# Optimization experiments

Hardware: AMD Instinct MI355X
Metric: run time of the kernel (lower is better)

Reference implementation:

```python
import jax, jax.numpy as jnp
import numpy as np

B, S, D = 2, 4096, 1024
H, HD = 16, 64
M = 512              # memseqlen == chunk size
L = 2 * M            # memory + chunk tokens
HID = 2816
EPS = 1e-5


def setup_inputs() -> dict:
    key = jax.random.key(0)
    ks = jax.random.split(key, 16)
    sc = 0.02
    return {
        "x": jax.random.normal(ks[0], (B, S, D), jnp.float32),
        "freqs_cos": jax.random.uniform(ks[1], (L, HD // 2), jnp.float32),
        "freqs_sin": jax.random.uniform(ks[2], (L, HD // 2), jnp.float32),
        "wq": jax.random.normal(ks[3], (D, D), jnp.float32) * sc,
        "wk": jax.random.normal(ks[4], (D, D), jnp.float32) * sc,
        "wv": jax.random.normal(ks[5], (D, D), jnp.float32) * sc,
        "wo": jax.random.normal(ks[6], (D, D), jnp.float32) * sc,
        "wm": jax.random.normal(ks[7], (D, D), jnp.float32) * sc,
        "wkm": jax.random.normal(ks[8], (D, D), jnp.float32) * sc,
        "wvm": jax.random.normal(ks[9], (D, D), jnp.float32) * sc,
        "w1": jax.random.normal(ks[10], (D, HID), jnp.float32) * sc,
        "w3": jax.random.normal(ks[11], (D, HID), jnp.float32) * sc,
        "w2": jax.random.normal(ks[12], (HID, D), jnp.float32) * sc,
        "ffn_norm_w": jnp.ones((D,), jnp.float32),
        "mem_norm_w": jnp.ones((D,), jnp.float32),
        "origin_mem": jnp.zeros((1, M, D), jnp.float32),
    }


def _rmsnorm(x, w):
    return x * jax.lax.rsqrt(jnp.mean(x * x, axis=-1, keepdims=True) + EPS) * w


def _rope(t, cos, sin):
    # t: (B, L, H, HD); cos/sin: (L, HD//2). Adjacent-pair complex rotation (llama2.c style).
    tr = t.reshape(*t.shape[:-1], HD // 2, 2)
    t_r, t_i = tr[..., 0], tr[..., 1]
    c = cos[None, :, None, :]
    s = sin[None, :, None, :]
    o_r = t_r * c - t_i * s
    o_i = t_r * s + t_i * c
    return jnp.stack([o_r, o_i], axis=-1).reshape(t.shape)


def reference(x, freqs_cos, freqs_sin, wq, wk, wv, wo, wm, wkm, wvm,
              w1, w2, w3, ffn_norm_w, mem_norm_w, origin_mem):
    bsz = x.shape[0]
    cos = freqs_cos[:L]
    sin = freqs_sin[:L]
    causal = jnp.tril(jnp.ones((L, L), dtype=bool))
    scale = 1.0 / jnp.sqrt(jnp.asarray(HD, x.dtype))

    def ffn(h):
        return (jax.nn.silu(h @ w1) * (h @ w3)) @ w2

    def step(om, subx):
        # token projections
        xq = (subx @ wq).reshape(bsz, M, H, HD)
        xk = (subx @ wk).reshape(bsz, M, H, HD)
        xv = (subx @ wv).reshape(bsz, M, H, HD)
        # memory glue: wm -> ffn residual -> rmsnorm
        om2 = om @ wm
        om2 = om2 + ffn(_rmsnorm(om2, ffn_norm_w))
        om2 = _rmsnorm(om2, mem_norm_w)
        # memory projections (source bug: mq is overwritten by mk; wqm unused)
        mk = (om2 @ wkm).reshape(bsz, M, H, HD)
        mv = (om2 @ wvm).reshape(bsz, M, H, HD)
        mq = mk
        q = jnp.concatenate([mq, xq], axis=1)  # (B, L, H, HD)
        k = jnp.concatenate([mk, xk], axis=1)
        v = jnp.concatenate([mv, xv], axis=1)
        q = _rope(q, cos, sin)
        k = _rope(k, cos, sin)
        # SDPA, causal over the concatenated length (n_rep == 1, repeat_kv is identity)
        qh = q.transpose(0, 2, 1, 3)
        kh = k.transpose(0, 2, 1, 3)
        vh = v.transpose(0, 2, 1, 3)
        scores = jnp.einsum('bhqd,bhkd->bhqk', qh, kh) * scale
        scores = jnp.where(causal, scores, jnp.finfo(scores.dtype).min)
        attn = jax.nn.softmax(scores, axis=-1)
        out = jnp.einsum('bhqk,bhkd->bhqd', attn, vh)
        out = out.transpose(0, 2, 1, 3).reshape(bsz, L, D)
        om_new = out[:, M:]  # token-part becomes next memory AND this chunk's output
        return om_new, om_new

    om0 = jnp.broadcast_to(origin_mem, (bsz, M, D))
    xc = x.reshape(bsz, S // M, M, D).transpose(1, 0, 2, 3)  # (n_chunks, B, M, D)
    _, outs = jax.lax.scan(step, om0, xc)
    out = outs.transpose(1, 0, 2, 3).reshape(bsz, S, D)
    return out @ wo
```

## Files before the change

### kernel.cpp

```cpp
#include <hip/hip_runtime.h>
#include <hip/hip_bf16.h>


#define D_    1024
#define H_    16
#define HD_   64
#define M_    512
#define L_    1024
#define HID_  2816
#define NSTEP 8

typedef __hip_bfloat16 bf16;
typedef _Float16 f16;
typedef __attribute__((ext_vector_type(8))) short short8;
typedef __attribute__((ext_vector_type(8))) _Float16 f16x8;
typedef __attribute__((ext_vector_type(4))) _Float16 f16x4;
typedef __attribute__((ext_vector_type(2))) _Float16 f16x2;
typedef __attribute__((ext_vector_type(4))) float floatx4;

__global__ void probe_dtype(const void* x, int* flag) {
  int lane = threadIdx.x;
  unsigned short v = ((const unsigned short*)x)[2 * lane];
  int e = (v >> 7) & 0xFF;
  bool sane = (e >= 100 && e <= 140);
  unsigned long long m = __ballot(sane);
  if (lane == 0) flag[0] = (__popcll(m) >= 40) ? 1 : 0;
}

__device__ __forceinline__ float load_any(const void* p, long i, int isbf) {
  return isbf ? __bfloat162float(((const bf16*)p)[i]) : ((const float*)p)[i];
}

__global__ __launch_bounds__(256) void transpose_cast(const void* in, bf16* out,
                                                      int K, int N, const int* flagp,
                                                      int stride, int off) {
  __shared__ float tile[32][33];
  int isbf = flagp[0];
  int tx = threadIdx.x & 31, ty = threadIdx.x >> 5;
  int n = blockIdx.x * 32 + tx;
#pragma unroll
  for (int i = 0; i < 4; i++) {
    int k = blockIdx.y * 32 + ty + i * 8;
    tile[ty + i * 8][tx] = load_any(in, (long)k * N + n, isbf);
  }
  __syncthreads();
  int k2 = blockIdx.y * 32 + tx;
#pragma unroll
  for (int i = 0; i < 4; i++) {
    int n2 = blockIdx.x * 32 + ty + i * 8;
    out[((long)n2 * stride + off) * K + k2] = __float2bfloat16(tile[tx][ty + i * 8]);
  }
}

__global__ __launch_bounds__(256) void transpose_cast_d7(
    const void* wq, const void* wk, const void* wv, const void* wm,
    const void* wkm, const void* wvm, const void* wo,
    bf16* wqkvT, bf16* wmT, bf16* wkmvmT, bf16* woT, const int* flagp) {
  __shared__ float tile[32][33];
  int z = blockIdx.z;
  const void* in;
  bf16* out;
  switch (z) {
    case 0: in = wq;  out = wqkvT;               break;
    case 1: in = wk;  out = wqkvT + 1048576;     break;
    case 2: in = wv;  out = wqkvT + 2 * 1048576; break;
    case 3: in = wm;  out = wmT;                 break;
    case 4: in = wkm; out = wkmvmT;              break;
    case 5: in = wvm; out = wkmvmT + 1048576;    break;
    default: in = wo; out = woT;                 break;
  }
  int isbf = flagp[0];
  int tx = threadIdx.x & 31, ty = threadIdx.x >> 5;
  int n = blockIdx.x * 32 + tx;
#pragma unroll
  for (int i = 0; i < 4; i++) {
    int k = blockIdx.y * 32 + ty + i * 8;
    tile[ty + i * 8][tx] = load_any(in, (long)k * 1024 + n, isbf);
  }
  __syncthreads();
  int k2 = blockIdx.y * 32 + tx;
#pragma unroll
  for (int i = 0; i < 4; i++) {
    int n2 = blockIdx.x * 32 + ty + i * 8;
    out[(long)n2 * 1024 + k2] = __float2bfloat16(tile[tx][ty + i * 8]);
  }
}

__global__ __launch_bounds__(256) void cast_to_bf16(const void* in, bf16* out, int n,
                                                    const int* flagp) {
  int i = blockIdx.x * 256 + threadIdx.x;
  if (i < n) out[i] = __float2bfloat16(load_any(in, i, flagp[0]));
}

__global__ __launch_bounds__(256) void cast_to_f32(const void* in, float* out, int n,
                                                   const int* flagp) {
  int i = blockIdx.x * 256 + threadIdx.x;
  if (i < n) out[i] = load_any(in, i, flagp[0]);
}

__global__ __launch_bounds__(256) void init_om(const void* in, bf16* om, const int* flagp) {
  int i = blockIdx.x * 256 + threadIdx.x;
  int rem = i & (M_ * D_ - 1);
  om[i] = __float2bfloat16(load_any(in, rem, flagp[0]));
}

#define GEMM64_BODY(Aptr, WTptr, Kld, kbeg, kend)                                   \
  __shared__ char smem[16384];                                                      \
  char* aT = smem;                                                                  \
  char* bT = smem + 8192;                                                           \
  int tid = threadIdx.x;                                                            \
  int wave = tid >> 6, lane = tid & 63;                                             \
  int wm_ = wave >> 1, wn_ = wave & 1;                                              \
  floatx4 acc[2][2] = {};                                                           \
  int q0 = tid, q1 = tid + 256;                                                     \
  int am0 = q0 >> 3, ac0 = q0 & 7;                                                  \
  int am1 = q1 >> 3, ac1 = q1 & 7;                                                  \
  long grow0 = R0 + am0, grow1 = R0 + am1;                                          \
  long bn0 = (long)(C0 + am0) * (Kld), bn1 = (long)(C0 + am1) * (Kld);              \
  int lofa0 = (am0 * 8 + (ac0 ^ (am0 & 7))) * 16;                                   \
  int lofa1 = (am1 * 8 + (ac1 ^ (am1 & 7))) * 16;                                   \
  for (int k0 = (kbeg); k0 < (kend); k0 += 64) {                                    \
    uint4 va0 = *(const uint4*)((Aptr) + grow0 * (Kld) + k0 + ac0 * 8);             \
    uint4 va1 = *(const uint4*)((Aptr) + grow1 * (Kld) + k0 + ac1 * 8);             \
    uint4 vb0 = *(const uint4*)((WTptr) + bn0 + k0 + ac0 * 8);                      \
    uint4 vb1 = *(const uint4*)((WTptr) + bn1 + k0 + ac1 * 8);                      \
    __syncthreads();                                                                \
    *(uint4*)(aT + lofa0) = va0;                                                    \
    *(uint4*)(aT + lofa1) = va1;                                                    \
    *(uint4*)(bT + lofa0) = vb0;                                                    \
    *(uint4*)(bT + lofa1) = vb1;                                                    \
    __syncthreads();                                                                \
    _Pragma("unroll") for (int kki = 0; kki < 2; ++kki) {                           \
      int cbase = kki * 4 + (lane >> 4);                                            \
      short8 af[2], bfr[2];                                                         \
      _Pragma("unroll") for (int i = 0; i < 2; ++i) {                               \
        int ml = wm_ * 32 + i * 16 + (lane & 15);                                   \
        af[i] = *(const short8*)(aT + (ml * 8 + (cbase ^ (ml & 7))) * 16);          \
        int nl = wn_ * 32 + i * 16 + (lane & 15);                                   \
        bfr[i] = *(const short8*)(bT + (nl * 8 + (cbase ^ (nl & 7))) * 16);         \
      }                                                                             \
      _Pragma("unroll") for (int i = 0; i < 2; ++i)                                 \
          _Pragma("unroll") for (int j = 0; j < 2; ++j) acc[i][j] =                 \
              __builtin_amdgcn_mfma_f32_16x16x32_bf16(af[i], bfr[j], acc[i][j],     \
                                                      0, 0, 0);                     \
    }                                                                               \
  }

__global__ __launch_bounds__(256) void gemm64_sk(
    const bf16* __restrict__ A, const bf16* __restrict__ WT,
    float* __restrict__ outP, int N, int Kfull, int Ksplit) {
  int C0 = blockIdx.x * 64, R0 = blockIdx.y * 64;
  int kb = blockIdx.z;
  float* out = outP + ((size_t)kb << 20);
  int kbeg = kb * Ksplit;
  GEMM64_BODY(A, WT, Kfull, kbeg, kbeg + Ksplit)
#pragma unroll
  for (int i = 0; i < 2; ++i)
#pragma unroll
    for (int j = 0; j < 2; ++j) {
      int row = R0 + wm_ * 32 + i * 16 + (lane >> 4) * 4;
      int col = C0 + wn_ * 32 + j * 16 + (lane & 15);
#pragma unroll
      for (int rg = 0; rg < 4; ++rg)
        out[(long)(row + rg) * N + col] = acc[i][j][rg];
    }
}

__global__ __launch_bounds__(256) void gemm64_kmvm(
    const bf16* __restrict__ A, const bf16* __restrict__ WT,
    const float* __restrict__ cosf, const float* __restrict__ sinf,
    f16* __restrict__ k_mem, f16* __restrict__ v_memT) {
  int C0 = blockIdx.x * 64, R0 = blockIdx.y * 64;
  GEMM64_BODY(A, WT, 1024, 0, 1024)
#pragma unroll
  for (int i = 0; i < 2; ++i)
#pragma unroll
    for (int j = 0; j < 2; ++j) {
      int row0 = R0 + wm_ * 32 + i * 16 + (lane >> 4) * 4;
      int col = C0 + wn_ * 32 + j * 16 + (lane & 15);
#pragma unroll
      for (int rg = 0; rg < 4; ++rg) {
        float v = acc[i][j][rg];
        int row = row0 + rg;
        int b = row >> 9, pos = row & 511;
        if (C0 < 1024) {
          float partner = __shfl_xor(v, 1);
          int ii = (col & 63) >> 1;
          float c = cosf[pos * 32 + ii], s = sinf[pos * 32 + ii];
          float o = (col & 1) ? (partner * s + v * c) : (v * c - partner * s);
          int bh = b * 16 + ((col >> 6) & 15);
          k_mem[((size_t)bh * 512 + pos) * 64 + (col & 63)] = (f16)o;
        } else {
          int d = col & 63;
          int bh = b * 16 + ((col - 1024) >> 6);
          v_memT[((size_t)bh * 64 + d) * 512 + pos] = (f16)v;
        }
      }
    }
}

__global__ __launch_bounds__(256) void gemm128(
    const bf16* __restrict__ A, const bf16* __restrict__ WT,
    void* __restrict__ out, const int* __restrict__ flagp,
    int N, int K, int out_mode,
    const float* __restrict__ cosf, const float* __restrict__ sinf,
    f16* __restrict__ q_x, f16* __restrict__ k_x, f16* __restrict__ v_xT) {
  __shared__ char smem[32768];
  int tid = threadIdx.x;
  int w = tid >> 6, lane = tid & 63;
  int C0 = blockIdx.x * 128, R0 = blockIdx.y * 128;
  int wm = (w >> 1) * 64, wn = (w & 1) * 64;
  int g = lane >> 4, n16 = lane & 15;
  floatx4 acc[4][4] = {};
  int lr = lane >> 3, lc = lane & 7;

  for (int k0 = 0; k0 < K; k0 += 64) {
    __syncthreads();
#pragma unroll
    for (int i = 0; i < 4; ++i) {
      int m = w * 32 + i * 8 + lr;
      int cg = lc ^ (m & 7);
      const bf16* ga = A + (size_t)(R0 + m) * K + k0 + cg * 8;
      const bf16* gb = WT + (size_t)(C0 + m) * K + k0 + cg * 8;
      __builtin_amdgcn_global_load_lds(
          (const __attribute__((address_space(1))) void*)ga,
          (__attribute__((address_space(3))) void*)(smem + (w * 32 + i * 8) * 128),
          16, 0, 0);
      __builtin_amdgcn_global_load_lds(
          (const __attribute__((address_space(1))) void*)gb,
          (__attribute__((address_space(3))) void*)(smem + 16384 + (w * 32 + i * 8) * 128),
          16, 0, 0);
    }
    __syncthreads();
#pragma unroll
    for (int kk = 0; kk < 2; ++kk) {
      short8 af[4], bfr[4];
#pragma unroll
      for (int i = 0; i < 4; ++i) {
        int ml = wm + i * 16 + n16;
        af[i] = *(const short8*)(smem + (ml * 8 + ((kk * 4 + g) ^ (ml & 7))) * 16);
        int nl = wn + i * 16 + n16;
        bfr[i] = *(const short8*)(smem + 16384 + (nl * 8 + ((kk * 4 + g) ^ (nl & 7))) * 16);
      }
#pragma unroll
      for (int i = 0; i < 4; ++i)
#pragma unroll
        for (int j = 0; j < 4; ++j)
          acc[i][j] = __builtin_amdgcn_mfma_f32_16x16x32_bf16(af[i], bfr[j], acc[i][j], 0, 0, 0);
    }
  }
  int isbf = flagp ? flagp[0] : 0;
#pragma unroll
  for (int i = 0; i < 4; ++i)
#pragma unroll
    for (int j = 0; j < 4; ++j) {
      int row = R0 + wm + i * 16 + g * 4;
      int col = C0 + wn + j * 16 + n16;
      if (out_mode == 4) {
        if (col < 2048) {
#pragma unroll
          for (int rg = 0; rg < 4; ++rg) {
            float v = acc[i][j][rg];
            float partner = __shfl_xor(v, 1);
            int r = row + rg;
            int m = r & 511, t = (r >> 9) & 7, b = r >> 12;
            int pos = 512 + m;
            int ii = (col & 63) >> 1;
            float c = cosf[pos * 32 + ii], s = sinf[pos * 32 + ii];
            float o = (col & 1) ? (partner * s + v * c) : (v * c - partner * s);
            int h = (col >> 6) & 15;
            size_t slab = (size_t)t * 32 + b * 16 + h;
            if (col < 1024)
              q_x[(slab * 512 + m) * 64 + (col & 63)] = (f16)(o * 0.125f);
            else
              k_x[(slab * 512 + m) * 64 + (col & 63)] = (f16)o;
          }
        } else {
          int r = row;
          int m = r & 511, t = (r >> 9) & 7, b = r >> 12;
          int d = col & 63, h = (col - 2048) >> 6;
          size_t slab = (size_t)t * 32 + b * 16 + h;
          f16x4 vv;
#pragma unroll
          for (int rg = 0; rg < 4; ++rg) vv[rg] = (f16)acc[i][j][rg];
          *(f16x4*)(v_xT + (slab * 64 + d) * 512 + m) = vv;
        }
        continue;
      }
#pragma unroll
      for (int rg = 0; rg < 4; ++rg) {
        float v = acc[i][j][rg];
        if (out_mode == 3) {
          float partner = __shfl_xor(v, 1);
          if ((n16 & 1) == 0) {
            float a = v;
            float s = a / (1.f + __expf(-a));
            ((bf16*)out)[(long)(row + rg) * HID_ + (col >> 1)] =
                __float2bfloat16(s * partner);
          }
          continue;
        }
        long off = (long)(row + rg) * N + col;
        if (out_mode == 0) ((float*)out)[off] = v;
        else if (out_mode == 1) ((f16*)out)[off] = (f16)v;
        else {
          if (isbf) ((bf16*)out)[off] = __float2bfloat16(v);
          else ((float*)out)[off] = v;
        }
      }
    }
}

__global__ __launch_bounds__(256) void rmsnorm_cast(const float* __restrict__ X,
                                                    const float* __restrict__ Wn,
                                                    bf16* __restrict__ Y,
                                                    const float* __restrict__ P,
                                                    int np,
                                                    float* __restrict__ sumout) {
  int row = blockIdx.x, tid = threadIdx.x;
  float vals[4], ss = 0.f;
#pragma unroll
  for (int i = 0; i < 4; i++) {
    int c = tid + i * 256;
    long idx = (long)row * D_ + c;
    float v = X ? X[idx] : 0.f;
    for (int k = 0; k < np; ++k) v += P[((size_t)k << 20) + idx];
    vals[i] = v;
    ss += v * v;
  }
#pragma unroll
  for (int off = 32; off; off >>= 1) ss += __shfl_xor(ss, off);
  __shared__ float wsum[4];
  int wv = tid >> 6, lane = tid & 63;
  if (lane == 0) wsum[wv] = ss;
  __syncthreads();
  ss = wsum[0] + wsum[1] + wsum[2] + wsum[3];
  float r = rsqrtf(ss * (1.0f / D_) + 1e-5f);
#pragma unroll
  for (int i = 0; i < 4; i++) {
    int c = tid + i * 256;
    if (sumout) sumout[(long)row * D_ + c] = vals[i];
    Y[(long)row * D_ + c] = __float2bfloat16(vals[i] * r * Wn[c]);
  }
}

__global__ __launch_bounds__(256) void attn_x(
    const f16* __restrict__ q_x, const f16* __restrict__ k_x,
    const f16* __restrict__ v_xT, float* __restrict__ OpartX,
    float* __restrict__ mpartX, float* __restrict__ lpartX) {
  __shared__ char smem[40960];
  int qt = blockIdx.x, bh = blockIdx.y, t = blockIdx.z;
  int tid = threadIdx.x;
  int w = tid >> 6, lane = tid & 63;
  int g = lane >> 4, n16 = lane & 15;
  int numc = qt + 1;
  int pos = 512 + qt * 64 + w * 16 + n16;
  size_t slab = (size_t)t * 32 + bh;

  f16x8 qf[2];
  {
    const f16* qp = q_x + (slab * 512 + qt * 64 + w * 16 + n16) * 64 + g * 8;
    qf[0] = *(const f16x8*)(qp);
    qf[1] = *(const f16x8*)(qp + 32);
  }
  floatx4 O[4] = {};
  float mrun = -1e30f, lrun = 0.f;

  int id0 = tid, id1 = tid + 256;
  int r0 = id0 >> 3, cc0 = id0 & 7;
  int r1 = id1 >> 3, cc1 = id1 & 7;
  int lof0 = ((r0 << 3) | (cc0 ^ (r0 & 7))) * 16;
  int lof1 = ((r1 << 3) | (cc1 ^ (r1 & 7))) * 16;

  uint4 kv0 = *(const uint4*)(k_x + (slab * 512 + r0) * 64 + cc0 * 8);
  uint4 kv1 = *(const uint4*)(k_x + (slab * 512 + r1) * 64 + cc1 * 8);
  uint4 vv0 = *(const uint4*)(v_xT + (slab * 64 + r0) * 512 + cc0 * 8);
  uint4 vv1 = *(const uint4*)(v_xT + (slab * 64 + r1) * 512 + cc1 * 8);

  char* Pw = smem + 32768 + w * 2048;

  for (int c = 0; c < numc; ++c) {
    char* Kb = smem + (c & 1) * 8192;
    char* Vb = smem + 16384 + (c & 1) * 8192;
    *(uint4*)(Kb + lof0) = kv0;
    *(uint4*)(Kb + lof1) = kv1;
    *(uint4*)(Vb + lof0) = vv0;
    *(uint4*)(Vb + lof1) = vv1;
    if (c + 1 < numc) {
      int ca = c + 1;
      kv0 = *(const uint4*)(k_x + (slab * 512 + ca * 64 + r0) * 64 + cc0 * 8);
      kv1 = *(const uint4*)(k_x + (slab * 512 + ca * 64 + r1) * 64 + cc1 * 8);
      vv0 = *(const uint4*)(v_xT + (slab * 64 + r0) * 512 + ca * 64 + cc0 * 8);
      vv1 = *(const uint4*)(v_xT + (slab * 64 + r1) * 512 + ca * 64 + cc1 * 8);
    }
    __syncthreads();

    floatx4 S[4] = {};
    __builtin_amdgcn_s_setprio(1);
#pragma unroll
    for (int kk = 0; kk < 2; ++kk) {
#pragma unroll
      for (int tn = 0; tn < 4; ++tn) {
        int row = tn * 16 + n16;
        f16x8 kf = *(const f16x8*)(Kb + (((row << 3) | ((kk * 4 + g) ^ (row & 7))) * 16));
        S[tn] = __builtin_amdgcn_mfma_f32_16x16x32_f16(kf, qf[kk], S[tn], 0, 0, 0);
      }
    }
    __builtin_amdgcn_s_setprio(0);
    if (c == numc - 1) {
      int kb = 512 + qt * 64;
#pragma unroll
      for (int tn = 0; tn < 4; ++tn)
#pragma unroll
        for (int r = 0; r < 4; ++r) {
          int key = kb + tn * 16 + g * 4 + r;
          if (key > pos) S[tn][r] = -1e30f;
        }
    }
    float smax = -1e30f;
#pragma unroll
    for (int tn = 0; tn < 4; ++tn)
#pragma unroll
      for (int r = 0; r < 4; ++r) smax = fmaxf(smax, S[tn][r]);
    smax = fmaxf(smax, __shfl_xor(smax, 16));
    smax = fmaxf(smax, __shfl_xor(smax, 32));
    float corr = 1.f;
    if (__any(smax > mrun + 8.f)) {
      float newm = fmaxf(mrun, smax);
      corr = __expf(mrun - newm);
      mrun = newm;
      float cr[4];
#pragma unroll
      for (int r = 0; r < 4; ++r) cr[r] = __shfl(corr, g * 4 + r);
#pragma unroll
      for (int dt = 0; dt < 4; ++dt)
#pragma unroll
        for (int r = 0; r < 4; ++r) O[dt][r] *= cr[r];
    }
    float lsum = 0.f;
#pragma unroll
    for (int tn = 0; tn < 4; ++tn) {
      f16x4 pk;
#pragma unroll
      for (int r = 0; r < 4; ++r) {
        float p = __expf(S[tn][r] - mrun);
        lsum += p;
        pk[r] = (f16)p;
      }
      int kapb = tn * 16 + g * 4;
      *(f16x4*)(Pw + (((n16 << 3) | ((kapb >> 3) ^ (n16 & 7))) * 16 + (kapb & 7) * 2)) = pk;
    }
    lsum += __shfl_xor(lsum, 16);
    lsum += __shfl_xor(lsum, 32);
    lrun = lrun * corr + lsum;
    __builtin_amdgcn_s_setprio(1);
#pragma unroll
    for (int kk = 0; kk < 2; ++kk) {
      f16x8 pf = *(const f16x8*)(Pw + (((n16 << 3) | ((kk * 4 + g) ^ (n16 & 7))) * 16));
#pragma unroll
      for (int dt = 0; dt < 4; ++dt) {
        int row = dt * 16 + n16;
        f16x8 vf =
            *(const f16x8*)(Vb + (((row << 3) | ((kk * 4 + g) ^ (row & 7))) * 16));
        O[dt] = __builtin_amdgcn_mfma_f32_16x16x32_f16(pf, vf, O[dt], 0, 0, 0);
      }
    }
    __builtin_amdgcn_s_setprio(0);
    __syncthreads();
  }
  int b = bh >> 4, h = bh & 15;
  if (g == 0) {
    int qq = qt * 64 + w * 16 + n16;
    mpartX[(size_t)t * 16384 + bh * 512 + qq] = mrun;
    lpartX[(size_t)t * 16384 + bh * 512 + qq] = lrun;
  }
#pragma unroll
  for (int dt = 0; dt < 4; ++dt)
#pragma unroll
    for (int r = 0; r < 4; ++r) {
      int qq = qt * 64 + w * 16 + g * 4 + r;
      size_t col = (size_t)h * 64 + dt * 16 + n16;
      OpartX[((size_t)t << 20) + (size_t)(b * 512 + qq) * 1024 + col] = O[dt][r];
    }
}

__global__ __launch_bounds__(256) void attn_mem(
    const f16* __restrict__ q_x, const f16* __restrict__ k_mem,
    const f16* __restrict__ v_memT, const float* __restrict__ OX,
    const float* __restrict__ mX, const float* __restrict__ lX,
    bf16* __restrict__ om_bf, bf16* __restrict__ outs_bf, int t) {
  __shared__ char smem[40960];
  int qt = blockIdx.x, bh = blockIdx.y;
  int tid = threadIdx.x;
  int w = tid >> 6, lane = tid & 63;
  int g = lane >> 4, n16 = lane & 15;
  size_t slab = (size_t)t * 32 + bh;

  f16x8 qf[2];
  {
    const f16* qp = q_x + (slab * 512 + qt * 64 + w * 16 + n16) * 64 + g * 8;
    qf[0] = *(const f16x8*)(qp);
    qf[1] = *(const f16x8*)(qp + 32);
  }
  floatx4 O[4] = {};
  float mrun = -1e30f, lrun = 0.f;

  int id0 = tid, id1 = tid + 256;
  int r0 = id0 >> 3, cc0 = id0 & 7;
  int r1 = id1 >> 3, cc1 = id1 & 7;
  int lof0 = ((r0 << 3) | (cc0 ^ (r0 & 7))) * 16;
  int lof1 = ((r1 << 3) | (cc1 ^ (r1 & 7))) * 16;

  uint4 kv0 = *(const uint4*)(k_mem + ((size_t)bh * 512 + r0) * 64 + cc0 * 8);
  uint4 kv1 = *(const uint4*)(k_mem + ((size_t)bh * 512 + r1) * 64 + cc1 * 8);
  uint4 vv0 = *(const uint4*)(v_memT + ((size_t)bh * 64 + r0) * 512 + cc0 * 8);
  uint4 vv1 = *(const uint4*)(v_memT + ((size_t)bh * 64 + r1) * 512 + cc1 * 8);

  char* Pw = smem + 32768 + w * 2048;

  for (int c = 0; c < 8; ++c) {
    char* Kb = smem + (c & 1) * 8192;
    char* Vb = smem + 16384 + (c & 1) * 8192;
    *(uint4*)(Kb + lof0) = kv0;
    *(uint4*)(Kb + lof1) = kv1;
    *(uint4*)(Vb + lof0) = vv0;
    *(uint4*)(Vb + lof1) = vv1;
    if (c + 1 < 8) {
      int ca = c + 1;
      kv0 = *(const uint4*)(k_mem + ((size_t)bh * 512 + ca * 64 + r0) * 64 + cc0 * 8);
      kv1 = *(const uint4*)(k_mem + ((size_t)bh * 512 + ca * 64 + r1) * 64 + cc1 * 8);
      vv0 = *(const uint4*)(v_memT + ((size_t)bh * 64 + r0) * 512 + ca * 64 + cc0 * 8);
      vv1 = *(const uint4*)(v_memT + ((size_t)bh * 64 + r1) * 512 + ca * 64 + cc1 * 8);
    }
    __syncthreads();

    floatx4 S[4] = {};
    __builtin_amdgcn_s_setprio(1);
#pragma unroll
    for (int kk = 0; kk < 2; ++kk) {
#pragma unroll
      for (int tn = 0; tn < 4; ++tn) {
        int row = tn * 16 + n16;
        f16x8 kf = *(const f16x8*)(Kb + (((row << 3) | ((kk * 4 + g) ^ (row & 7))) * 16));
        S[tn] = __builtin_amdgcn_mfma_f32_16x16x32_f16(kf, qf[kk], S[tn], 0, 0, 0);
      }
    }
    __builtin_amdgcn_s_setprio(0);
    float smax = -1e30f;
#pragma unroll
    for (int tn = 0; tn < 4; ++tn)
#pragma unroll
      for (int r = 0; r < 4; ++r) smax = fmaxf(smax, S[tn][r]);
    smax = fmaxf(smax, __shfl_xor(smax, 16));
    smax = fmaxf(smax, __shfl_xor(smax, 32));
    float corr = 1.f;
    if (__any(smax > mrun + 8.f)) {
      float newm = fmaxf(mrun, smax);
      corr = __expf(mrun - newm);
      mrun = newm;
      float cr[4];
#pragma unroll
      for (int r = 0; r < 4; ++r) cr[r] = __shfl(corr, g * 4 + r);
#pragma unroll
      for (int dt = 0; dt < 4; ++dt)
#pragma unroll
        for (int r = 0; r < 4; ++r) O[dt][r] *= cr[r];
    }
    float lsum = 0.f;
#pragma unroll
    for (int tn = 0; tn < 4; ++tn) {
      f16x4 pk;
#pragma unroll
      for (int r = 0; r < 4; ++r) {
        float p = __expf(S[tn][r] - mrun);
        lsum += p;
        pk[r] = (f16)p;
      }
      int kapb = tn * 16 + g * 4;
      *(f16x4*)(Pw + (((n16 << 3) | ((kapb >> 3) ^ (n16 & 7))) * 16 + (kapb & 7) * 2)) = pk;
    }
    lsum += __shfl_xor(lsum, 16);
    lsum += __shfl_xor(lsum, 32);
    lrun = lrun * corr + lsum;
    __builtin_amdgcn_s_setprio(1);
#pragma unroll
    for (int kk = 0; kk < 2; ++kk) {
      f16x8 pf = *(const f16x8*)(Pw + (((n16 << 3) | ((kk * 4 + g) ^ (n16 & 7))) * 16));
#pragma unroll
      for (int dt = 0; dt < 4; ++dt) {
        int row = dt * 16 + n16;
        f16x8 vf =
            *(const f16x8*)(Vb + (((row << 3) | ((kk * 4 + g) ^ (row & 7))) * 16));
        O[dt] = __builtin_amdgcn_mfma_f32_16x16x32_f16(pf, vf, O[dt], 0, 0, 0);
      }
    }
    __builtin_amdgcn_s_setprio(0);
    __syncthreads();
  }
  int b = bh >> 4, h = bh & 15;
  float a1[4], a2[4], rden[4];
  int qqr[4];
#pragma unroll
  for (int r = 0; r < 4; ++r) {
    float m1 = __shfl(mrun, g * 4 + r);
    float l1 = __shfl(lrun, g * 4 + r);
    qqr[r] = qt * 64 + w * 16 + g * 4 + r;
    int idx = bh * 512 + qqr[r];
    float m2 = mX[idx], l2 = lX[idx];
    float Mx = fmaxf(m1, m2);
    a1[r] = __expf(m1 - Mx);
    a2[r] = __expf(m2 - Mx);
    rden[r] = 1.f / (a1[r] * l1 + a2[r] * l2);
  }
#pragma unroll
  for (int dt = 0; dt < 4; ++dt)
#pragma unroll
    for (int r = 0; r < 4; ++r) {
      size_t col = (size_t)h * 64 + dt * 16 + n16;
      size_t rowoff = (size_t)(b * 512 + qqr[r]) * 1024 + col;
      float o2 = OX[rowoff];
      float v = (a1[r] * O[dt][r] + a2[r] * o2) * rden[r];
      bf16 bv = __float2bfloat16(v);
      om_bf[rowoff] = bv;
      outs_bf[((size_t)(b * 4096 + t * 512 + qqr[r])) * 1024 + col] = bv;
    }
}

extern "C" void kernel_launch(void* const* d_in, const int* in_sizes, int n_in,
                              void* d_out, int out_size, void* d_ws, size_t ws_size,
                              hipStream_t stream) {
  (void)in_sizes; (void)n_in; (void)out_size; (void)ws_size;
  const void* x   = d_in[0];
  const void* fc  = d_in[1];
  const void* fs  = d_in[2];
  const void* wq  = d_in[3];
  const void* wk  = d_in[4];
  const void* wv  = d_in[5];
  const void* wo  = d_in[6];
  const void* wm  = d_in[7];
  const void* wkm = d_in[8];
  const void* wvm = d_in[9];
  const void* w1  = d_in[10];
  const void* w3  = d_in[11];
  const void* w2  = d_in[12];
  const void* fnw = d_in[13];
  const void* mnw = d_in[14];
  const void* om0 = d_in[15];

  char* p = (char*)d_ws;
  auto alloc = [&](size_t bytes) -> char* {
    char* r = p;
    p += (bytes + 255) & ~(size_t)255;
    return r;
  };
  int*   flag    = (int*)alloc(256);
  bf16*  wqkvT   = (bf16*)alloc((size_t)3 * 1048576 * 2);
  bf16*  wmT     = (bf16*)alloc((size_t)1048576 * 2);
  bf16*  wkmvmT  = (bf16*)alloc((size_t)2 * 1048576 * 2);
  bf16*  w13T    = (bf16*)alloc((size_t)2 * 2883584 * 2);
  bf16*  w2T     = (bf16*)alloc((size_t)2883584 * 2);
  bf16*  woT     = (bf16*)alloc((size_t)1048576 * 2);
  bf16*  xb      = (bf16*)alloc((size_t)8388608 * 2);
  float* cosf    = (float*)alloc((size_t)32768 * 4);
  float* sinf    = (float*)alloc((size_t)32768 * 4);
  float* ffnw    = (float*)alloc((size_t)1024 * 4);
  float* memw    = (float*)alloc((size_t)1024 * 4);
  bf16*  om_bf   = (bf16*)alloc((size_t)1048576 * 2);
  bf16*  outs_bf = (bf16*)alloc((size_t)8388608 * 2);
  f16*   q_x     = (f16*)alloc((size_t)8 * 32 * 512 * 64 * 2);
  f16*   k_x     = (f16*)alloc((size_t)8 * 32 * 512 * 64 * 2);
  f16*   v_xT    = (f16*)alloc((size_t)8 * 32 * 512 * 64 * 2);
  float* OpartX  = (float*)alloc((size_t)8 * 1048576 * 4);
  float* mpartX  = (float*)alloc((size_t)8 * 16384 * 4);
  float* lpartX  = (float*)alloc((size_t)8 * 16384 * 4);
  float* om2a   = (float*)alloc((size_t)1048576 * 4);
  bf16*  h_bf   = (bf16*)alloc((size_t)1048576 * 2);
  bf16*  u_bf   = (bf16*)alloc((size_t)2883584 * 2);
  float* om2P   = (float*)alloc((size_t)2 * 1048576 * 4);
  bf16*  om2_bf = (bf16*)alloc((size_t)1048576 * 2);
  f16*   k_mem  = (f16*)alloc((size_t)1048576 * 2);
  f16*   v_memT = (f16*)alloc((size_t)1048576 * 2);

  dim3 tb(256);
  probe_dtype<<<1, 64, 0, stream>>>(x, flag);

  transpose_cast_d7<<<dim3(32, 32, 7), tb, 0, stream>>>(
      wq, wk, wv, wm, wkm, wvm, wo, wqkvT, wmT, wkmvmT, woT, flag);
  transpose_cast<<<dim3(88, 32), tb, 0, stream>>>(w1, w13T, 1024, 2816, flag, 2, 0);
  transpose_cast<<<dim3(88, 32), tb, 0, stream>>>(w3, w13T, 1024, 2816, flag, 2, 1);
  transpose_cast<<<dim3(32, 88), tb, 0, stream>>>(w2, w2T, 2816, 1024, flag, 1, 0);

  cast_to_bf16<<<32768, tb, 0, stream>>>(x, xb, 8388608, flag);
  cast_to_f32<<<128, tb, 0, stream>>>(fc, cosf, 32768, flag);
  cast_to_f32<<<128, tb, 0, stream>>>(fs, sinf, 32768, flag);
  cast_to_f32<<<4, tb, 0, stream>>>(fnw, ffnw, 1024, flag);
  cast_to_f32<<<4, tb, 0, stream>>>(mnw, memw, 1024, flag);
  init_om<<<4096, tb, 0, stream>>>(om0, om_bf, flag);

  gemm128<<<dim3(24, 64), tb, 0, stream>>>(xb, wqkvT, nullptr, flag, 3072, 1024, 4,
                                           cosf, sinf, q_x, k_x, v_xT);
  attn_x<<<dim3(8, 32, 8), tb, 0, stream>>>(q_x, k_x, v_xT, OpartX, mpartX, lpartX);

  for (int t = 0; t < NSTEP; ++t) {
    gemm64_sk<<<dim3(16, 16, 2), tb, 0, stream>>>(om_bf, wmT, om2P, 1024, 1024, 512);
    rmsnorm_cast<<<1024, tb, 0, stream>>>(nullptr, ffnw, h_bf, om2P, 2, om2a);
    gemm128<<<dim3(44, 8), tb, 0, stream>>>(h_bf, w13T, u_bf, flag, 5632, 1024, 3,
                                            nullptr, nullptr, nullptr, nullptr, nullptr);
    gemm64_sk<<<dim3(16, 16, 2), tb, 0, stream>>>(u_bf, w2T, om2P, 1024, 2816, 1408);
    rmsnorm_cast<<<1024, tb, 0, stream>>>(om2a, memw, om2_bf, om2P, 2, nullptr);
    gemm64_kmvm<<<dim3(32, 16), tb, 0, stream>>>(om2_bf, wkmvmT, cosf, sinf, k_mem, v_memT);
    attn_mem<<<dim3(8, 32), tb, 0, stream>>>(q_x, k_mem, v_memT,
                                             OpartX + ((size_t)t << 20),
                                             mpartX + (size_t)t * 16384,
                                             lpartX + (size_t)t * 16384,
                                             om_bf, outs_bf, t);
  }
  gemm128<<<dim3(8, 64), tb, 0, stream>>>(outs_bf, woT, d_out, flag, 1024, 1024, 2,
                                          nullptr, nullptr, nullptr, nullptr, nullptr);
}
```

Baseline: 1.100 ms.

## Split attn_mem into single-wave blocks with no block barriers

Reworks the memory-attention kernel so each block is one 64-lane wave handling 16 queries, with the grid growing from 256 to 1024 blocks. Each lane now loads 8 K and 8 V vectors per chunk, and both __syncthreads calls are dropped because one wave owns its LDS tile alone. The aim is more blocks to spread over the CUs and no barrier stalls. In exchange, K/V tiles are reloaded by four times as many blocks and each thread holds more registers, which could lower occupancy.

```diff
diff --git a/kernel.cpp b/kernel.cpp
--- a/kernel.cpp
+++ b/kernel.cpp
@@ -484,55 +484,59 @@
     }
 }
 
-__global__ __launch_bounds__(256) void attn_mem(
+__global__ __launch_bounds__(64) void attn_mem(
     const f16* __restrict__ q_x, const f16* __restrict__ k_mem,
     const f16* __restrict__ v_memT, const float* __restrict__ OX,
     const float* __restrict__ mX, const float* __restrict__ lX,
     bf16* __restrict__ om_bf, bf16* __restrict__ outs_bf, int t) {
-  __shared__ char smem[40960];
+  __shared__ char smem[34816];
   int qt = blockIdx.x, bh = blockIdx.y;
-  int tid = threadIdx.x;
-  int w = tid >> 6, lane = tid & 63;
+  int lane = threadIdx.x;
   int g = lane >> 4, n16 = lane & 15;
   size_t slab = (size_t)t * 32 + bh;
 
   f16x8 qf[2];
   {
-    const f16* qp = q_x + (slab * 512 + qt * 64 + w * 16 + n16) * 64 + g * 8;
+    const f16* qp = q_x + (slab * 512 + qt * 16 + n16) * 64 + g * 8;
     qf[0] = *(const f16x8*)(qp);
     qf[1] = *(const f16x8*)(qp + 32);
   }
   floatx4 O[4] = {};
   float mrun = -1e30f, lrun = 0.f;
 
-  int id0 = tid, id1 = tid + 256;
-  int r0 = id0 >> 3, cc0 = id0 & 7;
-  int r1 = id1 >> 3, cc1 = id1 & 7;
-  int lof0 = ((r0 << 3) | (cc0 ^ (r0 & 7))) * 16;
-  int lof1 = ((r1 << 3) | (cc1 ^ (r1 & 7))) * 16;
-
-  uint4 kv0 = *(const uint4*)(k_mem + ((size_t)bh * 512 + r0) * 64 + cc0 * 8);
-  uint4 kv1 = *(const uint4*)(k_mem + ((size_t)bh * 512 + r1) * 64 + cc1 * 8);
-  uint4 vv0 = *(const uint4*)(v_memT + ((size_t)bh * 64 + r0) * 512 + cc0 * 8);
-  uint4 vv1 = *(const uint4*)(v_memT + ((size_t)bh * 64 + r1) * 512 + cc1 * 8);
-
-  char* Pw = smem + 32768 + w * 2048;
+  int rr = lane >> 3, cc = lane & 7;
+  int lof[8];
+#pragma unroll
+  for (int j = 0; j < 8; ++j) {
+    int r = rr + 8 * j;
+    lof[j] = (r * 8 + (cc ^ (r & 7))) * 16;
+  }
+  uint4 kreg[8], vreg[8];
+#pragma unroll
+  for (int j = 0; j < 8; ++j) {
+    int r = rr + 8 * j;
+    kreg[j] = *(const uint4*)(k_mem + ((size_t)bh * 512 + r) * 64 + cc * 8);
+    vreg[j] = *(const uint4*)(v_memT + ((size_t)bh * 64 + r) * 512 + cc * 8);
+  }
+  char* Pw = smem + 32768;
 
   for (int c = 0; c < 8; ++c) {
     char* Kb = smem + (c & 1) * 8192;
     char* Vb = smem + 16384 + (c & 1) * 8192;
-    *(uint4*)(Kb + lof0) = kv0;
-    *(uint4*)(Kb + lof1) = kv1;
-    *(uint4*)(Vb + lof0) = vv0;
-    *(uint4*)(Vb + lof1) = vv1;
+#pragma unroll
+    for (int j = 0; j < 8; ++j) {
+      *(uint4*)(Kb + lof[j]) = kreg[j];
+      *(uint4*)(Vb + lof[j]) = vreg[j];
+    }
     if (c + 1 < 8) {
       int ca = c + 1;
-      kv0 = *(const uint4*)(k_mem + ((size_t)bh * 512 + ca * 64 + r0) * 64 + cc0 * 8);
-      kv1 = *(const uint4*)(k_mem + ((size_t)bh * 512 + ca * 64 + r1) * 64 + cc1 * 8);
-      vv0 = *(const uint4*)(v_memT + ((size_t)bh * 64 + r0) * 512 + ca * 64 + cc0 * 8);
-      vv1 = *(const uint4*)(v_memT + ((size_t)bh * 64 + r1) * 512 + ca * 64 + cc1 * 8);
-    }
-    __syncthreads();
+#pragma unroll
+      for (int j = 0; j < 8; ++j) {
+        int r = rr + 8 * j;
+        kreg[j] = *(const uint4*)(k_mem + ((size_t)bh * 512 + ca * 64 + r) * 64 + cc * 8);
+        vreg[j] = *(const uint4*)(v_memT + ((size_t)bh * 64 + r) * 512 + ca * 64 + cc * 8);
+      }
+    }
 
     floatx4 S[4] = {};
     __builtin_amdgcn_s_setprio(1);
@@ -595,7 +599,6 @@
       }
     }
     __builtin_amdgcn_s_setprio(0);
-    __syncthreads();
   }
   int b = bh >> 4, h = bh & 15;
   float a1[4], a2[4], rden[4];
@@ -604,7 +607,7 @@
   for (int r = 0; r < 4; ++r) {
     float m1 = __shfl(mrun, g * 4 + r);
     float l1 = __shfl(lrun, g * 4 + r);
-    qqr[r] = qt * 64 + w * 16 + g * 4 + r;
+    qqr[r] = qt * 16 + g * 4 + r;
     int idx = bh * 512 + qqr[r];
     float m2 = mX[idx], l2 = lX[idx];
     float Mx = fmaxf(m1, m2);
@@ -709,11 +712,11 @@
     gemm64_sk<<<dim3(16, 16, 2), tb, 0, stream>>>(u_bf, w2T, om2P, 1024, 2816, 1408);
     rmsnorm_cast<<<1024, tb, 0, stream>>>(om2a, memw, om2_bf, om2P, 2, nullptr);
     gemm64_kmvm<<<dim3(32, 16), tb, 0, stream>>>(om2_bf, wkmvmT, cosf, sinf, k_mem, v_memT);
-    attn_mem<<<dim3(8, 32), tb, 0, stream>>>(q_x, k_mem, v_memT,
-                                             OpartX + ((size_t)t << 20),
-                                             mpartX + (size_t)t * 16384,
-                                             lpartX + (size_t)t * 16384,
-                                             om_bf, outs_bf, t);
+    attn_mem<<<dim3(32, 32), dim3(64), 0, stream>>>(q_x, k_mem, v_memT,
+                                                    OpartX + ((size_t)t << 20),
+                                                    mpartX + (size_t)t * 16384,
+                                                    lpartX + (size_t)t * 16384,
+                                                    om_bf, outs_bf, t);
   }
   gemm128<<<dim3(8, 64), tb, 0, stream>>>(outs_bf, woT, d_out, flag, 1024, 1024, 2,
                                           nullptr, nullptr, nullptr, nullptr, nullptr);
```

Result: slower. 1.344 ms (+22.2%).
